# Optimization experiments

Hardware: AMD Instinct MI355X
Metric: run time of the kernel (lower is better)

## Reference

```python
import jax, jax.numpy as jnp
import numpy as np

N = 100000          # nodes
E = 3200000         # edges (avg degree 32)
F_IN = 128          # num_features
HID = 128           # hidden_channels
C = 8               # num_classes
G = 64              # graphs in batch
EPS = 1e-5


def setup_inputs() -> dict:
    key = jax.random.key(0)
    ks = jax.random.split(key, 10)
    x = jax.random.normal(ks[0], (N, F_IN), dtype=jnp.float32)
    edge_index = jax.random.randint(ks[1], (2, E), 0, N, dtype=jnp.int64)
    batch = jnp.sort(jax.random.randint(ks[2], (N,), 0, G, dtype=jnp.int64))
    # parameters
    glorot1 = float(np.sqrt(6.0 / (F_IN + HID)))
    W1 = jax.random.uniform(ks[3], (F_IN, HID), minval=-glorot1, maxval=glorot1, dtype=jnp.float32)
    conv1_bias = jnp.zeros((HID,), jnp.float32)
    bn_weight = jnp.ones((F_IN,), jnp.float32)
    bn_bias = jnp.zeros((F_IN,), jnp.float32)
    ln_weight = jnp.ones((HID,), jnp.float32)
    ln_bias = jnp.zeros((HID,), jnp.float32)
    glorot2 = float(np.sqrt(6.0 / (HID + C)))
    lin_W = jax.random.uniform(ks[4], (C, HID), minval=-glorot2, maxval=glorot2, dtype=jnp.float32)
    lin_b = jnp.zeros((C,), jnp.float32)
    return {"x": x, "edge_index": edge_index, "batch": batch,
            "bn_weight": bn_weight, "bn_bias": bn_bias,
            "W1": W1, "conv1_bias": conv1_bias,
            "ln_weight": ln_weight, "ln_bias": ln_bias,
            "lin_W": lin_W, "lin_b": lin_b}


def reference(x, edge_index, batch, bn_weight, bn_bias, W1, conv1_bias,
              ln_weight, ln_bias, lin_W, lin_b):
    n = x.shape[0]
    # BatchNorm1d over nodes (training-mode batch statistics, biased var)
    mu = x.mean(axis=0)
    var = x.var(axis=0)
    x = (x - mu) * jax.lax.rsqrt(var + EPS) * bn_weight + bn_bias
    # GCNConv: linear transform, add self-loops, symmetric normalization, scatter-add
    h = x @ W1                                   # [N, HID]
    loops = jnp.arange(n, dtype=edge_index.dtype)
    row = jnp.concatenate([edge_index[0], loops])  # source nodes
    col = jnp.concatenate([edge_index[1], loops])  # target nodes
    deg = jax.ops.segment_sum(jnp.ones_like(col, dtype=h.dtype), col, num_segments=N)
    dinv = jax.lax.rsqrt(deg)                    # deg >= 1 due to self-loops
    norm = dinv[row] * dinv[col]                 # [E+N]
    msg = h[row] * norm[:, None]                 # gather + scale
    h = jax.ops.segment_sum(msg, col, num_segments=N) + conv1_bias
    h = jax.nn.relu(h)
    # PyG LayerNorm, mode='graph', batch=None: normalize over the whole tensor
    h = h - h.mean()
    h = h * jax.lax.rsqrt(h.var() + EPS)
    h = h * ln_weight + ln_bias
    # global mean pool per graph
    counts = jax.ops.segment_sum(jnp.ones((n,), h.dtype), batch, num_segments=G)
    sums = jax.ops.segment_sum(h, batch, num_segments=G)
    g = sums / jnp.maximum(counts, 1.0)[:, None]  # [G, HID]
    return g @ lin_W.T + lin_b                    # [G, C]
```

## Files before the change

kernel.cpp:

```cpp
#include <hip/hip_runtime.h>

#define NN 100000
#define NE 3200000
#define F 128
#define NG 64
#define NC 8
#define EPSF 1e-5f

#define AGG_BLOCKS 25000
#define LDSTRIDE 136
#define BN_BLOCKS 1024

#define NBK 256
#define BNODES 391
#define BCAP 14336
#define CHUNK 4096
#define P1_BLOCKS ((NE + CHUNK - 1) / CHUNK)

typedef __attribute__((ext_vector_type(8))) short bf16x8;
typedef __attribute__((ext_vector_type(4))) float f32x4;
typedef _Float16 f16x2 __attribute__((ext_vector_type(2)));

union U32H2 { unsigned int u; f16x2 h; };
__device__ __forceinline__ f16x2 asH2(unsigned int u) { U32H2 c; c.u = u; return c.h; }
__device__ __forceinline__ unsigned int asU32(f16x2 h) { U32H2 c; c.h = h; return c.u; }

__device__ __forceinline__ unsigned short f2bf(float f) {
    unsigned int u = __float_as_uint(f);
    u = u + 0x7FFFu + ((u >> 16) & 1u);
    return (unsigned short)(u >> 16);
}
__device__ __forceinline__ unsigned short f2h_bits(float f) {
    union { _Float16 h; unsigned short u; } c;
    c.h = (_Float16)f;
    return c.u;
}

__global__ __launch_bounds__(256) void bn_bucket_k(const float* __restrict__ x,
                                                   float* __restrict__ part, int n, int rpb,
                                                   const int* __restrict__ ei,
                                                   int* __restrict__ bcur,
                                                   unsigned int* __restrict__ bbuf) {
    __shared__ float shf[512];
    __shared__ int cntl[NBK];
    __shared__ int basel[NBK];
    __shared__ int gbase[NBK];
    __shared__ unsigned int ent[CHUNK];
    __shared__ unsigned char bid[CHUNK];
    int tid = threadIdx.x;
    if (blockIdx.x < BN_BLOCKS) {
        int col = tid & 127, half = tid >> 7;
        int r0 = blockIdx.x * rpb, r1 = min(n, r0 + rpb);
        float s = 0.f, ss = 0.f;
        for (int r = r0 + half; r < r1; r += 2) {
            float v = x[(size_t)r * F + col];
            s += v; ss += v * v;
        }
        shf[tid] = s; shf[256 + tid] = ss;
        __syncthreads();
        if (half == 0) {
            part[blockIdx.x * 256 + col]       = shf[col] + shf[col + 128];
            part[blockIdx.x * 256 + 128 + col] = shf[256 + col] + shf[256 + col + 128];
        }
        return;
    }
    int e0 = (blockIdx.x - BN_BLOCKS) * CHUNK;
    int ecnt = min(NE - e0, CHUNK);
    cntl[tid] = 0;
    __syncthreads();
    int myr[16], myc[16], myl[16];
    #pragma unroll
    for (int k = 0; k < 16; ++k) {
        int i = tid + k * 256;
        if (i < ecnt) {
            int r = ei[e0 + i];
            int c = ei[NE + e0 + i];
            myr[k] = r; myc[k] = c;
            myl[k] = atomicAdd(&cntl[(unsigned)c / BNODES], 1);
        } else { myr[k] = -1; myc[k] = 0; myl[k] = 0; }
    }
    __syncthreads();
    int myv = cntl[tid];
    basel[tid] = myv;
    __syncthreads();
    for (int o = 1; o < 256; o <<= 1) {
        int t = (tid >= o) ? basel[tid - o] : 0;
        __syncthreads();
        basel[tid] += t;
        __syncthreads();
    }
    basel[tid] -= myv;
    gbase[tid] = atomicAdd(&bcur[tid], myv);
    __syncthreads();
    #pragma unroll
    for (int k = 0; k < 16; ++k) {
        if (myr[k] >= 0) {
            int b = (unsigned)myc[k] / BNODES;
            int s = basel[b] + myl[k];
            ent[s] = ((unsigned)myr[k] << 9) | (unsigned)(myc[k] - b * BNODES);
            bid[s] = (unsigned char)b;
        }
    }
    __syncthreads();
    for (int s = tid; s < ecnt; s += 256) {
        unsigned int v = ent[s];
        int b = bid[s];
        int idx = s - basel[b] + gbase[b];
        if (idx < BCAP) bbuf[(size_t)b * BCAP + idx] = v;
    }
}

__global__ void finalize_both_k(const float* __restrict__ part,
                                const float* __restrict__ bnw, const float* __restrict__ bnb,
                                float* __restrict__ scale, float* __restrict__ shift, int n,
                                const int* __restrict__ bcur, int* __restrict__ bbase,
                                int* __restrict__ offs, float* __restrict__ gsum) {
    int tid = threadIdx.x;
    if (blockIdx.x < 128) {
        int col = blockIdx.x;
        float s = 0.f, ss = 0.f;
        #pragma unroll
        for (int i = 0; i < 4; ++i) {
            int b = tid + i * 256;
            s  += part[b * 256 + col];
            ss += part[b * 256 + 128 + col];
        }
        __shared__ float shs[256], shss[256];
        shs[tid] = s; shss[tid] = ss;
        __syncthreads();
        for (int o = 128; o > 0; o >>= 1) {
            if (tid < o) { shs[tid] += shs[tid + o]; shss[tid] += shss[tid + o]; }
            __syncthreads();
        }
        if (tid == 0) {
            float mu  = shs[0] / (float)n;
            float var = shss[0] / (float)n - mu * mu;
            float rstd = rsqrtf(var + EPSF);
            float sc = bnw[col] * rstd;
            scale[col] = sc;
            shift[col] = bnb[col] - mu * sc;
        }
        return;
    }
    if (blockIdx.x == 129) {
        for (int i = tid; i < NG * F; i += 256) gsum[i] = 0.f;
        return;
    }
    __shared__ int s[256];
    int v = bcur[tid];
    s[tid] = v;
    __syncthreads();
    for (int o = 1; o < 256; o <<= 1) {
        int t = (tid >= o) ? s[tid - o] : 0;
        __syncthreads();
        s[tid] += t;
        __syncthreads();
    }
    bbase[tid] = s[tid] - v;
    if (tid == 255) offs[NN] = s[255];
}

__global__ void prep_csr_k(const float* __restrict__ W1, const float* __restrict__ scale,
                           const float* __restrict__ shift,
                           unsigned short* __restrict__ WpT, float* __restrict__ S,
                           const unsigned int* __restrict__ bbuf, const int* __restrict__ bcur,
                           const int* __restrict__ bbase,
                           int* __restrict__ offs, float* __restrict__ dinv,
                           int* __restrict__ srow) {
    int tid = threadIdx.x;
    if (blockIdx.x < 64) {
        int idx = blockIdx.x * 256 + tid;
        int k = idx >> 7, j = idx & 127;
        WpT[j * F + k] = f2bf(scale[k] * W1[idx]);
        return;
    }
    if (blockIdx.x < 192) {
        int j = blockIdx.x - 64;
        __shared__ float sh[256];
        sh[tid] = (tid < 128) ? shift[tid] * W1[tid * F + j] : 0.f;
        __syncthreads();
        for (int o = 128; o > 0; o >>= 1) {
            if (tid < o) sh[tid] += sh[tid + o];
            __syncthreads();
        }
        if (tid == 0) S[j] = sh[0];
        return;
    }
    int b = blockIdx.x - 192;
    __shared__ int h0[512], hA[512], hB[512];
    h0[tid] = 0; h0[tid + 256] = 0;
    __syncthreads();
    int m = min(bcur[b], BCAP);
    for (int i = tid; i < m; i += 256)
        atomicAdd(&h0[bbuf[(size_t)b * BCAP + i] & 511u], 1);
    __syncthreads();
    hA[tid] = h0[tid]; hA[tid + 256] = h0[tid + 256];
    __syncthreads();
    int* src = hA; int* dst = hB;
    for (int o = 1; o < 512; o <<= 1) {
        int i0 = tid, i1 = tid + 256;
        dst[i0] = src[i0] + ((i0 >= o) ? src[i0 - o] : 0);
        dst[i1] = src[i1] + ((i1 >= o) ? src[i1 - o] : 0);
        __syncthreads();
        int* tmp = src; src = dst; dst = tmp;
    }
    int nbase = b * BNODES;
    int base = bbase[b];
    int lim = min(BNODES, NN - nbase);
    for (int i = tid; i < lim; i += 256) {
        int d = h0[i];
        offs[nbase + i] = base + src[i] - d;
        dinv[nbase + i] = rsqrtf((float)d + 1.0f);
    }
    dst[tid] = src[tid] - h0[tid];
    dst[tid + 256] = src[tid + 256] - h0[tid + 256];
    __syncthreads();
    for (int i = tid; i < m; i += 256) {
        unsigned int v = bbuf[(size_t)b * BCAP + i];
        int dstl = (int)(v & 511u);
        int pos = base + atomicAdd(&dst[dstl], 1);
        srow[pos] = (int)(v >> 9);
    }
}

__global__ __launch_bounds__(256) void gemm_k(const float* __restrict__ x,
                                              const unsigned short* __restrict__ WpT,
                                              const float* __restrict__ S,
                                              const float* __restrict__ dinv,
                                              unsigned short* __restrict__ hf, int n) {
    __shared__ unsigned short wt[128 * LDSTRIDE];
    __shared__ unsigned short xt[64 * LDSTRIDE];
    int tid = threadIdx.x;
    int row0 = blockIdx.x * 64;
    for (int i = tid; i < 2048; i += 256) {
        int r = i >> 4, c = (i & 15) * 8;
        uint4 v = *(const uint4*)&WpT[r * F + c];
        *(uint4*)&wt[r * LDSTRIDE + c] = v;
    }
    for (int i = tid; i < 2048; i += 256) {
        int r = i >> 5, c = (i & 31) * 4;
        float4 v = make_float4(0.f, 0.f, 0.f, 0.f);
        if (row0 + r < n) v = *(const float4*)&x[(size_t)(row0 + r) * F + c];
        unsigned int p0 = (unsigned int)f2bf(v.x) | ((unsigned int)f2bf(v.y) << 16);
        unsigned int p1 = (unsigned int)f2bf(v.z) | ((unsigned int)f2bf(v.w) << 16);
        *(uint2*)&xt[r * LDSTRIDE + c] = make_uint2(p0, p1);
    }
    __syncthreads();
    int wv = tid >> 6, lane = tid & 63;
    int lm = lane & 15, lk = lane >> 4;
    bf16x8 afrag[4];
    #pragma unroll
    for (int kk = 0; kk < 4; ++kk)
        afrag[kk] = *(bf16x8*)&xt[(wv * 16 + lm) * LDSTRIDE + kk * 32 + lk * 8];
    float dv[4];
    #pragma unroll
    for (int j = 0; j < 4; ++j) {
        int r = row0 + wv * 16 + lk * 4 + j;
        dv[j] = (r < n) ? dinv[r] : 1.0f;
    }
    #pragma unroll
    for (int nt = 0; nt < 8; ++nt) {
        float sv = S[nt * 16 + lm];
        f32x4 acc = {sv, sv, sv, sv};
        #pragma unroll
        for (int kk = 0; kk < 4; ++kk) {
            bf16x8 b = *(bf16x8*)&wt[(nt * 16 + lm) * LDSTRIDE + kk * 32 + lk * 8];
            acc = __builtin_amdgcn_mfma_f32_16x16x32_bf16(afrag[kk], b, acc, 0, 0, 0);
        }
        #pragma unroll
        for (int j = 0; j < 4; ++j) {
            int r = row0 + wv * 16 + lk * 4 + j;
            if (r < n) hf[(size_t)r * F + nt * 16 + lm] = f2h_bits(acc[j] * dv[j]);
        }
    }
}

__global__ __launch_bounds__(256) void agg_k(const uint4* __restrict__ hb4,
                                             const int* __restrict__ srow,
                                             const int* __restrict__ offs,
                                             const float* __restrict__ dinv,
                                             const float* __restrict__ bias,
                                             uint4* __restrict__ h2p4,
                                             float* __restrict__ lnpart, int n) {
    int lane = threadIdx.x & 63, wv = threadIdx.x >> 6;
    int node = blockIdx.x * 4 + wv;
    int cg = lane & 15;
    int sub = lane >> 4;
    float s_part = 0.f, ss_part = 0.f;
    if (node < n) {
        int st = offs[node], en = offs[node + 1];
        float di = dinv[node];
        f16x2 a0 = {0.f16, 0.f16}, a1 = a0, a2 = a0, a3 = a0;
        if (sub == 0) {
            uint4 qs = hb4[(size_t)node * 16 + cg];
            a0 += asH2(qs.x); a1 += asH2(qs.y); a2 += asH2(qs.z); a3 += asH2(qs.w);
        }
        const uint4 qz = make_uint4(0u, 0u, 0u, 0u);
        for (int base = st; base < en; base += 64) {
            int m = en - base; if (m > 64) m = 64;
            int sv = (lane < m) ? srow[base + lane] : 0;
            int nq = (m + 3) >> 2;
            int k = 0;
            for (; k + 4 <= nq; k += 4) {
                int i0 = 4 * k + sub, i1 = i0 + 4, i2 = i0 + 8, i3 = i0 + 12;
                int sr0 = __shfl(sv, i0), sr1 = __shfl(sv, i1);
                int sr2 = __shfl(sv, i2), sr3 = __shfl(sv, i3);
                bool v0 = i0 < m, v1 = i1 < m, v2 = i2 < m, v3 = i3 < m;
                uint4 q0 = hb4[(size_t)(v0 ? sr0 : node) * 16 + cg];
                uint4 q1 = hb4[(size_t)(v1 ? sr1 : node) * 16 + cg];
                uint4 q2 = hb4[(size_t)(v2 ? sr2 : node) * 16 + cg];
                uint4 q3 = hb4[(size_t)(v3 ? sr3 : node) * 16 + cg];
                if (!v0) q0 = qz;
                if (!v1) q1 = qz;
                if (!v2) q2 = qz;
                if (!v3) q3 = qz;
                a0 += asH2(q0.x); a1 += asH2(q0.y); a2 += asH2(q0.z); a3 += asH2(q0.w);
                a0 += asH2(q1.x); a1 += asH2(q1.y); a2 += asH2(q1.z); a3 += asH2(q1.w);
                a0 += asH2(q2.x); a1 += asH2(q2.y); a2 += asH2(q2.z); a3 += asH2(q2.w);
                a0 += asH2(q3.x); a1 += asH2(q3.y); a2 += asH2(q3.z); a3 += asH2(q3.w);
            }
            for (; k < nq; ++k) {
                int i0 = 4 * k + sub;
                int sr0 = __shfl(sv, i0);
                bool v0 = i0 < m;
                uint4 q0 = hb4[(size_t)(v0 ? sr0 : node) * 16 + cg];
                if (!v0) q0 = qz;
                a0 += asH2(q0.x); a1 += asH2(q0.y); a2 += asH2(q0.z); a3 += asH2(q0.w);
            }
        }
        a0 += asH2((unsigned int)__shfl_xor((int)asU32(a0), 16));
        a1 += asH2((unsigned int)__shfl_xor((int)asU32(a1), 16));
        a2 += asH2((unsigned int)__shfl_xor((int)asU32(a2), 16));
        a3 += asH2((unsigned int)__shfl_xor((int)asU32(a3), 16));
        a0 += asH2((unsigned int)__shfl_xor((int)asU32(a0), 32));
        a1 += asH2((unsigned int)__shfl_xor((int)asU32(a1), 32));
        a2 += asH2((unsigned int)__shfl_xor((int)asU32(a2), 32));
        a3 += asH2((unsigned int)__shfl_xor((int)asU32(a3), 32));
        float acc[8] = {(float)a0[0], (float)a0[1], (float)a1[0], (float)a1[1],
                        (float)a2[0], (float)a2[1], (float)a3[0], (float)a3[1]};
        float4 b0 = *(const float4*)&bias[cg * 8];
        float4 b1 = *(const float4*)&bias[cg * 8 + 4];
        float bv[8] = {b0.x, b0.y, b0.z, b0.w, b1.x, b1.y, b1.z, b1.w};
        float r[8];
        #pragma unroll
        for (int j = 0; j < 8; ++j) r[j] = fmaxf(fmaf(acc[j], di, bv[j]), 0.f);
        if (sub == 0) {
            uint4 p;
            p.x = asU32(f16x2{(_Float16)r[0], (_Float16)r[1]});
            p.y = asU32(f16x2{(_Float16)r[2], (_Float16)r[3]});
            p.z = asU32(f16x2{(_Float16)r[4], (_Float16)r[5]});
            p.w = asU32(f16x2{(_Float16)r[6], (_Float16)r[7]});
            h2p4[(size_t)node * 16 + cg] = p;
            #pragma unroll
            for (int j = 0; j < 8; ++j) {
                s_part += r[j];
                ss_part += r[j] * r[j];
            }
        }
    }
    __shared__ float sh[512];
    sh[threadIdx.x] = s_part; sh[256 + threadIdx.x] = ss_part;
    __syncthreads();
    for (int o = 128; o > 0; o >>= 1) {
        if (threadIdx.x < o) {
            sh[threadIdx.x] += sh[threadIdx.x + o];
            sh[256 + threadIdx.x] += sh[256 + threadIdx.x + o];
        }
        __syncthreads();
    }
    if (threadIdx.x == 0) {
        lnpart[blockIdx.x * 2]     = sh[0];
        lnpart[blockIdx.x * 2 + 1] = sh[256];
    }
}

__global__ void pool1_k(const unsigned int* __restrict__ h2p, const int* __restrict__ batch,
                        float* __restrict__ gsum, int n) {
    int tid = threadIdx.x, cp = tid & 63, half = tid >> 6;
    int n0 = blockIdx.x * 256, n1 = min(n, n0 + 256);
    int r = n0 + half;
    if (r >= n1) return;
    int gcur = batch[r];
    float a0 = 0.f, a1 = 0.f;
    for (; r < n1; r += 4) {
        int g = batch[r];
        f16x2 hp = asH2(h2p[(size_t)r * 64 + cp]);
        if (g != gcur) {
            atomicAdd(&gsum[gcur * F + cp * 2], a0);
            atomicAdd(&gsum[gcur * F + cp * 2 + 1], a1);
            a0 = a1 = 0.f; gcur = g;
        }
        a0 += (float)hp[0];
        a1 += (float)hp[1];
    }
    atomicAdd(&gsum[gcur * F + cp * 2], a0);
    atomicAdd(&gsum[gcur * F + cp * 2 + 1], a1);
}

__global__ void pool2_k(const float* __restrict__ gsum, const int* __restrict__ batch,
                        const float* __restrict__ lnpart, int nb,
                        const float* __restrict__ lnw, const float* __restrict__ lnb,
                        const float* __restrict__ linW, const float* __restrict__ linb,
                        float* __restrict__ out, int n) {
    int g = blockIdx.x, tid = threadIdx.x;
    __shared__ double shd[512];
    __shared__ float lnmu, lnrs;
    double s = 0.0, ss = 0.0;
    for (int i = tid; i < nb; i += 256) {
        s  += (double)lnpart[2 * i];
        ss += (double)lnpart[2 * i + 1];
    }
    shd[tid] = s; shd[256 + tid] = ss;
    __syncthreads();
    for (int o = 128; o > 0; o >>= 1) {
        if (tid < o) { shd[tid] += shd[tid + o]; shd[256 + tid] += shd[256 + tid + o]; }
        __syncthreads();
    }
    __shared__ int bounds[2];
    if (tid == 0) {
        double cnt = (double)NN * (double)F;
        double mu = shd[0] / cnt;
        double var = shd[256] / cnt - mu * mu;
        lnmu = (float)mu;
        lnrs = (float)(1.0 / sqrt(var + (double)EPSF));
    }
    if (tid < 2) {
        int target = g + tid;
        int lo = 0, hi = n;
        while (lo < hi) {
            int mid = (lo + hi) >> 1;
            if (batch[mid] < target) lo = mid + 1; else hi = mid;
        }
        bounds[tid] = lo;
    }
    __syncthreads();
    int cg = bounds[1] - bounds[0];
    __shared__ float vals[128];
    if (tid < 128) {
        float v = 0.f;
        if (cg > 0) {
            float m = gsum[g * F + tid] / (float)cg;
            v = (m - lnmu) * lnrs * lnw[tid] + lnb[tid];
        }
        vals[tid] = v;
    }
    __syncthreads();
    if (tid < NC) {
        float o = linb[tid];
        for (int k = 0; k < F; ++k) o = fmaf(vals[k], linW[tid * F + k], o);
        out[g * NC + tid] = o;
    }
}

extern "C" void kernel_launch(void* const* d_in, const int* in_sizes, int n_in,
                              void* d_out, int out_size, void* d_ws, size_t ws_size,
                              hipStream_t stream) {
    const float* x     = (const float*)d_in[0];
    const int*   ei    = (const int*)d_in[1];
    const int*   batch = (const int*)d_in[2];
    const float* bnw   = (const float*)d_in[3];
    const float* bnb   = (const float*)d_in[4];
    const float* W1    = (const float*)d_in[5];
    const float* cbias = (const float*)d_in[6];
    const float* lnw   = (const float*)d_in[7];
    const float* lnb   = (const float*)d_in[8];
    const float* linW  = (const float*)d_in[9];
    const float* linb  = (const float*)d_in[10];
    float* out = (float*)d_out;

    char* w = (char*)d_ws;
    size_t used = 0;
    auto alloc = [&](size_t bytes) {
        char* p = w;
        size_t pad = (bytes + 255) & ~(size_t)255;
        w += pad;
        used += pad;
        return p;
    };
    size_t bucket_bytes = (size_t)NBK * BCAP * 4;
    size_t hf_bytes     = (size_t)NN * F * 2;
    char* regionA = (char*)alloc(bucket_bytes > hf_bytes ? bucket_bytes : hf_bytes);
    unsigned int*   bbuf = (unsigned int*)regionA;
    unsigned short* hf   = (unsigned short*)regionA;

    unsigned int* h2p = (unsigned int*)alloc((size_t)NN * F * 2);
    int*   srow    = (int*)alloc((size_t)NE * 4);
    int*   offs    = (int*)alloc((size_t)(NN + 1) * 4);
    float* dinv    = (float*)alloc((size_t)NN * 4);
    int*   bcur    = (int*)alloc(NBK * 4);
    int*   bbase   = (int*)alloc(NBK * 4);
    float* bnpart  = (float*)alloc((size_t)BN_BLOCKS * 256 * 4);
    float* scale   = (float*)alloc(512);
    float* shift   = (float*)alloc(512);
    unsigned short* WpT = (unsigned short*)alloc(128 * 128 * 2);
    float* Svec    = (float*)alloc(512);
    float* lnpart  = (float*)alloc((size_t)AGG_BLOCKS * 2 * 4);
    float* gsum    = (float*)alloc((size_t)NG * F * 4);

    if (used > ws_size) {
        hipMemsetAsync(d_out, 0, (size_t)out_size * 4, stream);
        return;
    }

    hipMemsetAsync(bcur, 0, NBK * 4, stream);

    int rpb = (NN + BN_BLOCKS - 1) / BN_BLOCKS;
    bn_bucket_k<<<BN_BLOCKS + P1_BLOCKS, 256, 0, stream>>>(x, bnpart, NN, rpb, ei, bcur, bbuf);
    finalize_both_k<<<130, 256, 0, stream>>>(bnpart, bnw, bnb, scale, shift, NN,
                                             bcur, bbase, offs, gsum);
    prep_csr_k<<<448, 256, 0, stream>>>(W1, scale, shift, WpT, Svec,
                                        bbuf, bcur, bbase, offs, dinv, srow);

    gemm_k<<<(NN + 63) / 64, 256, 0, stream>>>(x, WpT, Svec, dinv, hf, NN);
    agg_k<<<AGG_BLOCKS, 256, 0, stream>>>((const uint4*)hf, srow, offs, dinv,
                                          cbias, (uint4*)h2p, lnpart, NN);
    pool1_k<<<(NN + 255) / 256, 256, 0, stream>>>(h2p, batch, gsum, NN);
    pool2_k<<<NG, 256, 0, stream>>>(gsum, batch, lnpart, AGG_BLOCKS,
                                    lnw, lnb, linW, linb, out, NN);
}
```

Measured before the change: 266.0 us.

## Overlap CSR scatter with GEMM and fold LayerNorm reduction into pooling

The CSR edge-scatter phase moves out of the histogram/prefix kernel into a combined launch with the GEMM. The first 256 blocks scatter source indices into the CSR array while the remaining blocks run the bf16 MFMA transform, so the two phases can overlap. The LayerNorm partial sums are now reduced inside pool1 using wavefront shuffles and float atomics. This stops all 64 pool2 blocks from each re-reducing 50k partials in double precision, and pool2 now launches 128 threads. The bucket buffer is re-aliased onto h2p instead of hf to avoid a conflict, and the global statistics are now accumulated in float rather than double.

```diff
diff --git a/kernel.cpp b/kernel.cpp
--- a/kernel.cpp
+++ b/kernel.cpp
@@ -16,6 +16,7 @@
 #define BCAP 14336
 #define CHUNK 4096
 #define P1_BLOCKS ((NE + CHUNK - 1) / CHUNK)
+#define GEMM_BLOCKS ((NN + 63) / 64)
 
 typedef __attribute__((ext_vector_type(8))) short bf16x8;
 typedef __attribute__((ext_vector_type(4))) float f32x4;
@@ -114,7 +115,8 @@
                                 const float* __restrict__ bnw, const float* __restrict__ bnb,
                                 float* __restrict__ scale, float* __restrict__ shift, int n,
                                 const int* __restrict__ bcur, int* __restrict__ bbase,
-                                int* __restrict__ offs, float* __restrict__ gsum) {
+                                int* __restrict__ offs, float* __restrict__ gsum,
+                                float* __restrict__ lnsum) {
     int tid = threadIdx.x;
     if (blockIdx.x < 128) {
         int col = blockIdx.x;
@@ -144,6 +146,7 @@
     }
     if (blockIdx.x == 129) {
         for (int i = tid; i < NG * F; i += 256) gsum[i] = 0.f;
+        if (tid < 2) lnsum[tid] = 0.f;
         return;
     }
     __shared__ int s[256];
@@ -160,13 +163,12 @@
     if (tid == 255) offs[NN] = s[255];
 }
 
-__global__ void prep_csr_k(const float* __restrict__ W1, const float* __restrict__ scale,
-                           const float* __restrict__ shift,
-                           unsigned short* __restrict__ WpT, float* __restrict__ S,
-                           const unsigned int* __restrict__ bbuf, const int* __restrict__ bcur,
-                           const int* __restrict__ bbase,
-                           int* __restrict__ offs, float* __restrict__ dinv,
-                           int* __restrict__ srow) {
+__global__ void prep_hist_k(const float* __restrict__ W1, const float* __restrict__ scale,
+                            const float* __restrict__ shift,
+                            unsigned short* __restrict__ WpT, float* __restrict__ S,
+                            const unsigned int* __restrict__ bbuf, const int* __restrict__ bcur,
+                            const int* __restrict__ bbase,
+                            int* __restrict__ offs, float* __restrict__ dinv) {
     int tid = threadIdx.x;
     if (blockIdx.x < 64) {
         int idx = blockIdx.x * 256 + tid;
@@ -212,26 +214,34 @@
         offs[nbase + i] = base + src[i] - d;
         dinv[nbase + i] = rsqrtf((float)d + 1.0f);
     }
-    dst[tid] = src[tid] - h0[tid];
-    dst[tid + 256] = src[tid + 256] - h0[tid + 256];
-    __syncthreads();
-    for (int i = tid; i < m; i += 256) {
-        unsigned int v = bbuf[(size_t)b * BCAP + i];
-        int dstl = (int)(v & 511u);
-        int pos = base + atomicAdd(&dst[dstl], 1);
-        srow[pos] = (int)(v >> 9);
-    }
-}
-
-__global__ __launch_bounds__(256) void gemm_k(const float* __restrict__ x,
-                                              const unsigned short* __restrict__ WpT,
-                                              const float* __restrict__ S,
-                                              const float* __restrict__ dinv,
-                                              unsigned short* __restrict__ hf, int n) {
-    __shared__ unsigned short wt[128 * LDSTRIDE];
-    __shared__ unsigned short xt[64 * LDSTRIDE];
+}
+
+__global__ __launch_bounds__(256) void scatter_gemm_k(
+        const unsigned int* __restrict__ bbuf, const int* __restrict__ bcur,
+        const int* __restrict__ offs, int* __restrict__ srow,
+        const float* __restrict__ x, const unsigned short* __restrict__ WpT,
+        const float* __restrict__ S, const float* __restrict__ dinv,
+        unsigned short* __restrict__ hf, int n) {
+    __shared__ __align__(16) char smem[128 * LDSTRIDE * 2 + 64 * LDSTRIDE * 2];
     int tid = threadIdx.x;
-    int row0 = blockIdx.x * 64;
+    if (blockIdx.x < NBK) {
+        int b = blockIdx.x;
+        int* cur = (int*)smem;
+        for (int i = tid; i < BNODES; i += 256) cur[i] = 0;
+        __syncthreads();
+        int nbase = b * BNODES;
+        int m = min(bcur[b], BCAP);
+        for (int i = tid; i < m; i += 256) {
+            unsigned int v = bbuf[(size_t)b * BCAP + i];
+            int dstl = (int)(v & 511u);
+            int pos = offs[nbase + dstl] + atomicAdd(&cur[dstl], 1);
+            srow[pos] = (int)(v >> 9);
+        }
+        return;
+    }
+    unsigned short* wt = (unsigned short*)smem;
+    unsigned short* xt = (unsigned short*)(smem + 128 * LDSTRIDE * 2);
+    int row0 = (blockIdx.x - NBK) * 64;
     for (int i = tid; i < 2048; i += 256) {
         int r = i >> 4, c = (i & 15) * 8;
         uint4 v = *(const uint4*)&WpT[r * F + c];
@@ -375,8 +385,27 @@
 }
 
 __global__ void pool1_k(const unsigned int* __restrict__ h2p, const int* __restrict__ batch,
-                        float* __restrict__ gsum, int n) {
-    int tid = threadIdx.x, cp = tid & 63, half = tid >> 6;
+                        float* __restrict__ gsum, float* __restrict__ lnsum, int n) {
+    int tid = threadIdx.x;
+    if (tid < 64) {
+        int e = blockIdx.x * 64 + tid;
+        float s = 0.f, ss = 0.f;
+        if (e < AGG_BLOCKS) {
+            const float* lp = lnsum + 2;
+            s  = lp[2 * e];
+            ss = lp[2 * e + 1];
+        }
+        #pragma unroll
+        for (int o = 32; o > 0; o >>= 1) {
+            s  += __shfl_down(s, o);
+            ss += __shfl_down(ss, o);
+        }
+        if (tid == 0) {
+            atomicAdd(&lnsum[0], s);
+            atomicAdd(&lnsum[1], ss);
+        }
+    }
+    int cp = tid & 63, half = tid >> 6;
     int n0 = blockIdx.x * 256, n1 = min(n, n0 + 256);
     int r = n0 + half;
     if (r >= n1) return;
@@ -398,31 +427,19 @@
 }
 
 __global__ void pool2_k(const float* __restrict__ gsum, const int* __restrict__ batch,
-                        const float* __restrict__ lnpart, int nb,
+                        const float* __restrict__ lnsum,
                         const float* __restrict__ lnw, const float* __restrict__ lnb,
                         const float* __restrict__ linW, const float* __restrict__ linb,
                         float* __restrict__ out, int n) {
     int g = blockIdx.x, tid = threadIdx.x;
-    __shared__ double shd[512];
     __shared__ float lnmu, lnrs;
-    double s = 0.0, ss = 0.0;
-    for (int i = tid; i < nb; i += 256) {
-        s  += (double)lnpart[2 * i];
-        ss += (double)lnpart[2 * i + 1];
-    }
-    shd[tid] = s; shd[256 + tid] = ss;
-    __syncthreads();
-    for (int o = 128; o > 0; o >>= 1) {
-        if (tid < o) { shd[tid] += shd[tid + o]; shd[256 + tid] += shd[256 + tid + o]; }
-        __syncthreads();
-    }
     __shared__ int bounds[2];
     if (tid == 0) {
-        double cnt = (double)NN * (double)F;
-        double mu = shd[0] / cnt;
-        double var = shd[256] / cnt - mu * mu;
-        lnmu = (float)mu;
-        lnrs = (float)(1.0 / sqrt(var + (double)EPSF));
+        float cnt = (float)NN * (float)F;
+        float mu = lnsum[0] / cnt;
+        float var = lnsum[1] / cnt - mu * mu;
+        lnmu = mu;
+        lnrs = rsqrtf(var + EPSF);
     }
     if (tid < 2) {
         int target = g + tid;
@@ -478,12 +495,12 @@
         return p;
     };
     size_t bucket_bytes = (size_t)NBK * BCAP * 4;
-    size_t hf_bytes     = (size_t)NN * F * 2;
-    char* regionA = (char*)alloc(bucket_bytes > hf_bytes ? bucket_bytes : hf_bytes);
-    unsigned int*   bbuf = (unsigned int*)regionA;
-    unsigned short* hf   = (unsigned short*)regionA;
-
-    unsigned int* h2p = (unsigned int*)alloc((size_t)NN * F * 2);
+    size_t h2p_bytes    = (size_t)NN * F * 2;
+    char* regionA = (char*)alloc(bucket_bytes > h2p_bytes ? bucket_bytes : h2p_bytes);
+    unsigned int* bbuf = (unsigned int*)regionA;
+    unsigned int* h2p  = (unsigned int*)regionA;
+
+    unsigned short* hf = (unsigned short*)alloc((size_t)NN * F * 2);
     int*   srow    = (int*)alloc((size_t)NE * 4);
     int*   offs    = (int*)alloc((size_t)(NN + 1) * 4);
     float* dinv    = (float*)alloc((size_t)NN * 4);
@@ -494,7 +511,8 @@
     float* shift   = (float*)alloc(512);
     unsigned short* WpT = (unsigned short*)alloc(128 * 128 * 2);
     float* Svec    = (float*)alloc(512);
-    float* lnpart  = (float*)alloc((size_t)AGG_BLOCKS * 2 * 4);
+    float* lnsum   = (float*)alloc(8 + (size_t)AGG_BLOCKS * 2 * 4);
+    float* lnpart  = lnsum + 2;
     float* gsum    = (float*)alloc((size_t)NG * F * 4);
 
     if (used > ws_size) {
@@ -507,14 +525,13 @@
     int rpb = (NN + BN_BLOCKS - 1) / BN_BLOCKS;
     bn_bucket_k<<<BN_BLOCKS + P1_BLOCKS, 256, 0, stream>>>(x, bnpart, NN, rpb, ei, bcur, bbuf);
     finalize_both_k<<<130, 256, 0, stream>>>(bnpart, bnw, bnb, scale, shift, NN,
-                                             bcur, bbase, offs, gsum);
-    prep_csr_k<<<448, 256, 0, stream>>>(W1, scale, shift, WpT, Svec,
-                                        bbuf, bcur, bbase, offs, dinv, srow);
-
-    gemm_k<<<(NN + 63) / 64, 256, 0, stream>>>(x, WpT, Svec, dinv, hf, NN);
+                                             bcur, bbase, offs, gsum, lnsum);
+    prep_hist_k<<<448, 256, 0, stream>>>(W1, scale, shift, WpT, Svec,
+                                         bbuf, bcur, bbase, offs, dinv);
+    scatter_gemm_k<<<NBK + GEMM_BLOCKS, 256, 0, stream>>>(bbuf, bcur, offs, srow,
+                                                          x, WpT, Svec, dinv, hf, NN);
     agg_k<<<AGG_BLOCKS, 256, 0, stream>>>((const uint4*)hf, srow, offs, dinv,
                                           cbias, (uint4*)h2p, lnpart, NN);
-    pool1_k<<<(NN + 255) / 256, 256, 0, stream>>>(h2p, batch, gsum, NN);
-    pool2_k<<<NG, 256, 0, stream>>>(gsum, batch, lnpart, AGG_BLOCKS,
-                                    lnw, lnb, linW, linb, out, NN);
-}
+    pool1_k<<<(NN + 255) / 256, 256, 0, stream>>>(h2p, batch, gsum, lnsum, NN);
+    pool2_k<<<NG, 128, 0, stream>>>(gsum, batch, lnsum, lnw, lnb, linW, linb, out, NN);
+}
```

Result: faster. 244.5 us (-8.1%).
